# Kernel tuning notes

Measured on AMD Instinct MI355X. Metric: run time of the kernel, lower is better.

## Reference

```python
import jax, jax.numpy as jnp
import numpy as np

B, T, I, O = 64, 1024, 512, 512
EPS = 1e-5


def setup_inputs() -> dict:
    key = jax.random.key(0)
    k1, k2 = jax.random.split(key)
    x = jax.random.normal(k1, (B, T, I), dtype=jnp.float32)
    W = jax.random.normal(k2, (4 * O, I + O), dtype=jnp.float32) * 0.02
    gamma = jnp.ones((4, O), dtype=jnp.float32)
    beta = jnp.zeros((4, O), dtype=jnp.float32)
    init_hx = jnp.zeros((1, O), dtype=jnp.float32)
    init_cx = jnp.zeros((1, O), dtype=jnp.float32)
    return {"x": x, "W": W, "gamma": gamma, "beta": beta,
            "init_hx": init_hx, "init_cx": init_cx}


def reference(x, W, gamma, beta, init_hx, init_cx):
    b = x.shape[0]
    o = init_hx.shape[-1]

    def step(carry, xt):
        h, c = carry
        # fused gate projection: [B, I+O] @ [I+O, 4O] -> [B, 4, O]
        z = jnp.concatenate([xt, h], axis=-1) @ W.T
        z = z.reshape(b, 4, o)
        # LayerNorm over the last TWO dims (gate axis + feature axis), per torch nn.LayerNorm([4, O])
        mu = jnp.mean(z, axis=(-2, -1), keepdims=True)
        var = jnp.var(z, axis=(-2, -1), keepdims=True)
        zn = (z - mu) * jax.lax.rsqrt(var + EPS) * gamma + beta
        gates = jax.nn.sigmoid(zn[:, :3])  # f, i, o gates
        f_g, i_g, o_g = gates[:, 0], gates[:, 1], gates[:, 2]
        h_state = jax.nn.gelu(zn[:, 3], approximate=False)  # dropout = identity (eval)
        c_new = f_g * c + i_g * h_state
        h_new = o_g * c_new
        return (h_new, c_new), h_new

    h0 = jnp.broadcast_to(init_hx, (b, o))
    c0 = jnp.broadcast_to(init_cx, (b, o))
    x_t = jnp.swapaxes(x, 0, 1)  # [T, B, I]
    _, hs = jax.lax.scan(step, (h0, c0), x_t)
    return jnp.swapaxes(hs, 0, 1)  # [B, T, O]
```

## Files before the change

### kernel.cpp

```cpp
#include <hip/hip_runtime.h>
#include <math.h>

#define B_  64
#define T_  1024
#define I_  512
#define O_  512
#define NZ  2048
#define KW  1024
#define EPS 1e-5f

#define SREC 32
#define OSL  16

typedef short bf8_t  __attribute__((ext_vector_type(8)));
typedef float f32x4  __attribute__((ext_vector_type(4)));

__device__ __forceinline__ unsigned short f2bf(float f) {
  union { float f; unsigned u; } v; v.f = f;
  unsigned r = v.u + 0x7FFFu + ((v.u >> 16) & 1u);
  return (unsigned short)(r >> 16);
}
__device__ __forceinline__ float bf2f(unsigned short b) {
  union { unsigned u; float f; } v; v.u = ((unsigned)b) << 16;
  return v.f;
}

__global__ __launch_bounds__(256) void init_all(
    const float* __restrict__ init_hx,
    unsigned short* __restrict__ h, unsigned* __restrict__ sync) {
  int idx = blockIdx.x * 256 + threadIdx.x;
  if (idx < 2048) sync[idx] = 0u;
  if (idx < B_ * O_) h[idx] = f2bf(init_hx[idx & (O_ - 1)]);
}

__global__ __launch_bounds__(256) void wx_bf16(
    const float* __restrict__ W, unsigned short* __restrict__ Wbf) {
  int idx = blockIdx.x * 256 + threadIdx.x;
  int n  = idx >> 7;
  int k4 = (idx & 127) * 4;
  float4 v = *(const float4*)(W + (size_t)n * KW + k4);
  unsigned short* d = Wbf + (size_t)n * 512 + k4;
  d[0] = f2bf(v.x); d[1] = f2bf(v.y); d[2] = f2bf(v.z); d[3] = f2bf(v.w);
}

__global__ __launch_bounds__(256) void zx_gemm(
    const float* __restrict__ x, const unsigned short* __restrict__ Wbf,
    unsigned short* __restrict__ zx) {
  __shared__ unsigned short xl[64 * 520];

  const int tid  = threadIdx.x;
  const int w    = tid >> 6;
  const int lane = tid & 63;
  const int q    = lane >> 4;
  const int col  = lane & 15;
  const int m0   = blockIdx.x * 64;

  for (int e4 = tid; e4 < 64 * 128; e4 += 256) {
    int r  = e4 >> 7;
    int k4 = (e4 & 127) * 4;
    float4 v = *(const float4*)(x + (size_t)(m0 + r) * I_ + k4);
    unsigned short* d = &xl[r * 520 + k4];
    d[0] = f2bf(v.x); d[1] = f2bf(v.y); d[2] = f2bf(v.z); d[3] = f2bf(v.w);
  }
  __syncthreads();

  const unsigned short* __restrict__ arow = &xl[(16 * w + col) * 520];

  for (int nblk = 0; nblk < 32; ++nblk) {
    const int n0 = nblk * 64;
    f32x4 acc[4];
    #pragma unroll
    for (int i = 0; i < 4; ++i) acc[i] = (f32x4){0.f, 0.f, 0.f, 0.f};

    #pragma unroll
    for (int ks = 0; ks < 16; ++ks) {
      const int k0 = ks * 32 + q * 8;
      bf8_t af = *(const bf8_t*)(arow + k0);
      #pragma unroll
      for (int nt = 0; nt < 4; ++nt) {
        bf8_t bfr = *(const bf8_t*)(Wbf + (size_t)(n0 + nt * 16 + col) * 512 + k0);
        acc[nt] = __builtin_amdgcn_mfma_f32_16x16x32_bf16(af, bfr, acc[nt], 0, 0, 0);
      }
    }
    #pragma unroll
    for (int nt = 0; nt < 4; ++nt)
      #pragma unroll
      for (int r = 0; r < 4; ++r) {
        int m = m0 + 16 * w + 4 * q + r;
        zx[(size_t)m * NZ + n0 + nt * 16 + col] = f2bf(acc[nt][r]);
      }
  }
}

__global__ __launch_bounds__(256) void lstm_rec(
    const float* __restrict__ W, const float* __restrict__ gamma,
    const float* __restrict__ beta, const float* __restrict__ init_cx,
    const unsigned short* __restrict__ zx, unsigned short* __restrict__ h,
    unsigned long long* __restrict__ part8, float* __restrict__ out,
    unsigned* __restrict__ flags) {

  __shared__ unsigned short whlds[64 * 520];

  const int tid  = threadIdx.x;
  const int w    = tid >> 6;
  const int lane = tid & 63;
  const int q    = lane >> 4;
  const int col  = lane & 15;
  const int s    = blockIdx.x;
  const int o    = s * OSL + col;

  for (int e4 = tid; e4 < 64 * 128; e4 += 256) {
    int r  = e4 >> 7;
    int k4 = (e4 & 127) * 4;
    int g  = r >> 4, np = r & 15;
    const float4 v =
        *(const float4*)(W + (size_t)(512 * g + OSL * s + np) * KW + I_ + k4);
    unsigned short* d = &whlds[r * 520 + k4];
    d[0] = f2bf(v.x); d[1] = f2bf(v.y); d[2] = f2bf(v.z); d[3] = f2bf(v.w);
  }

  float gma[4], bta[4], c_reg[4];
  #pragma unroll
  for (int g = 0; g < 4; ++g) { gma[g] = gamma[g * O_ + o]; bta[g] = beta[g * O_ + o]; }
  { float c0 = init_cx[o];
    #pragma unroll
    for (int r = 0; r < 4; ++r) c_reg[r] = c0; }

  unsigned short zxl[16];
  #pragma unroll
  for (int g = 0; g < 4; ++g)
    #pragma unroll
    for (int r = 0; r < 4; ++r) {
      int b = 16 * w + 4 * q + r;
      zxl[g * 4 + r] = zx[((size_t)b * T_ + 0) * NZ + g * O_ + OSL * s + col];
    }

  __syncthreads();

  for (int t = 0; t < T_; ++t) {
    unsigned long long araw[32];
    const unsigned short* hrow = h + (16 * w + col) * O_;
    #pragma unroll
    for (int ks = 0; ks < 16; ++ks) {
      const unsigned long long* p =
          (const unsigned long long*)(hrow + ks * 32 + q * 8);
      araw[2 * ks]     = __hip_atomic_load(p,     __ATOMIC_RELAXED, __HIP_MEMORY_SCOPE_AGENT);
      araw[2 * ks + 1] = __hip_atomic_load(p + 1, __ATOMIC_RELAXED, __HIP_MEMORY_SCOPE_AGENT);
    }

    f32x4 acc[4];
    #pragma unroll
    for (int g = 0; g < 4; ++g) acc[g] = (f32x4){0.f, 0.f, 0.f, 0.f};

    #pragma unroll
    for (int ks = 0; ks < 16; ++ks) {
      union { unsigned long long u[2]; bf8_t v; } au;
      au.u[0] = araw[2 * ks]; au.u[1] = araw[2 * ks + 1];
      #pragma unroll
      for (int g = 0; g < 4; ++g) {
        bf8_t bfr = *(const bf8_t*)(&whlds[(g * 16 + col) * 520 + ks * 32 + q * 8]);
        acc[g] = __builtin_amdgcn_mfma_f32_16x16x32_bf16(au.v, bfr, acc[g], 0, 0, 0);
      }
    }

    float z[16];
    float s1[4], s2[4];
    #pragma unroll
    for (int r = 0; r < 4; ++r) { s1[r] = 0.f; s2[r] = 0.f; }
    #pragma unroll
    for (int g = 0; g < 4; ++g)
      #pragma unroll
      for (int r = 0; r < 4; ++r) {
        float zv = acc[g][r] + bf2f(zxl[g * 4 + r]);
        z[g * 4 + r] = zv;
        s1[r] += zv;
        s2[r] += zv * zv;
      }
    #pragma unroll
    for (int m = 1; m < 16; m <<= 1) {
      #pragma unroll
      for (int r = 0; r < 4; ++r) {
        s1[r] += __shfl_xor(s1[r], m, 64);
        s2[r] += __shfl_xor(s2[r], m, 64);
      }
    }
    if (col == 0) {
      #pragma unroll
      for (int r = 0; r < 4; ++r) {
        int b = 16 * w + 4 * q + r;
        union { float f[2]; unsigned long long u; } pv;
        pv.f[0] = s1[r]; pv.f[1] = s2[r];
        __hip_atomic_store(&part8[(size_t)s * 64 + b], pv.u,
                           __ATOMIC_RELAXED, __HIP_MEMORY_SCOPE_AGENT);
      }
    }

    __syncthreads();
    {
      const unsigned tgt = 2u * (unsigned)t + 1u;
      if (tid == 0)
        __hip_atomic_store(&flags[s * 16], tgt,
                           __ATOMIC_RELAXED, __HIP_MEMORY_SCOPE_AGENT);
      const unsigned* fp = &flags[(tid & 31) * 16];
      while (__hip_atomic_load(fp, __ATOMIC_RELAXED, __HIP_MEMORY_SCOPE_AGENT) < tgt) {}
    }

    float S1 = 0.f, S2 = 0.f;
    {
      const int brow = 16 * w + (lane & 15);
      const int sbase = (lane >> 4) * 8;
      #pragma unroll
      for (int i = 0; i < 8; ++i) {
        union { float f[2]; unsigned long long u; } pv;
        pv.u = __hip_atomic_load(&part8[(size_t)(sbase + i) * 64 + brow],
                                 __ATOMIC_RELAXED, __HIP_MEMORY_SCOPE_AGENT);
        S1 += pv.f[0]; S2 += pv.f[1];
      }
    }
    S1 += __shfl_xor(S1, 16, 64); S2 += __shfl_xor(S2, 16, 64);
    S1 += __shfl_xor(S1, 32, 64); S2 += __shfl_xor(S2, 32, 64);
    float mean_l = S1 * (1.f / NZ);
    float rstd_l = rsqrtf(S2 * (1.f / NZ) - mean_l * mean_l + EPS);

    float hnl[4];
    #pragma unroll
    for (int r = 0; r < 4; ++r) {
      int b = 16 * w + 4 * q + r;
      float mean = __shfl(mean_l, 4 * q + r, 64);
      float rstd = __shfl(rstd_l, 4 * q + r, 64);
      float zn0 = (z[0 * 4 + r] - mean) * rstd * gma[0] + bta[0];
      float zn1 = (z[1 * 4 + r] - mean) * rstd * gma[1] + bta[1];
      float zn2 = (z[2 * 4 + r] - mean) * rstd * gma[2] + bta[2];
      float zn3 = (z[3 * 4 + r] - mean) * rstd * gma[3] + bta[3];
      float fg = 1.f / (1.f + expf(-zn0));
      float ig = 1.f / (1.f + expf(-zn1));
      float og = 1.f / (1.f + expf(-zn2));
      float gg = 0.5f * zn3 * (1.f + erff(zn3 * 0.70710678118654752f));
      float cn = fg * c_reg[r] + ig * gg;
      float hn = og * cn;
      c_reg[r] = cn;
      hnl[r] = hn;
      __hip_atomic_store(&h[b * O_ + o], f2bf(hn),
                         __ATOMIC_RELAXED, __HIP_MEMORY_SCOPE_AGENT);
    }

    if (t + 1 < T_) {
      __syncthreads();
      const unsigned tgt = 2u * (unsigned)t + 2u;
      if (tid == 0)
        __hip_atomic_store(&flags[s * 16], tgt,
                           __ATOMIC_RELAXED, __HIP_MEMORY_SCOPE_AGENT);
      #pragma unroll
      for (int r = 0; r < 4; ++r) {
        int b = 16 * w + 4 * q + r;
        out[((size_t)b * T_ + t) * O_ + o] = hnl[r];
      }
      #pragma unroll
      for (int g = 0; g < 4; ++g)
        #pragma unroll
        for (int r = 0; r < 4; ++r) {
          int b = 16 * w + 4 * q + r;
          zxl[g * 4 + r] =
              zx[((size_t)b * T_ + (t + 1)) * NZ + g * O_ + OSL * s + col];
        }
      const unsigned* fp = &flags[(tid & 31) * 16];
      while (__hip_atomic_load(fp, __ATOMIC_RELAXED, __HIP_MEMORY_SCOPE_AGENT) < tgt) {}
    } else {
      #pragma unroll
      for (int r = 0; r < 4; ++r) {
        int b = 16 * w + 4 * q + r;
        out[((size_t)b * T_ + t) * O_ + o] = hnl[r];
      }
    }
  }
}

extern "C" void kernel_launch(void* const* d_in, const int* in_sizes, int n_in,
                              void* d_out, int out_size, void* d_ws, size_t ws_size,
                              hipStream_t stream) {
  const float* x       = (const float*)d_in[0];
  const float* W       = (const float*)d_in[1];
  const float* gamma   = (const float*)d_in[2];
  const float* beta    = (const float*)d_in[3];
  const float* init_hx = (const float*)d_in[4];
  const float* init_cx = (const float*)d_in[5];
  float* out = (float*)d_out;
  (void)in_sizes; (void)n_in; (void)out_size; (void)ws_size;

  char* ws = (char*)d_ws;
  unsigned*           flags = (unsigned*)(ws);
  unsigned long long* part8 = (unsigned long long*)(ws + 8192);
  unsigned short*     h     = (unsigned short*)(ws + 32768);
  unsigned short*     Wbf   = (unsigned short*)(ws + (1 << 20));
  unsigned short*     zx    = (unsigned short*)(ws + (4 << 20));

  init_all<<<128, 256, 0, stream>>>(init_hx, h, flags);
  wx_bf16<<<1024, 256, 0, stream>>>(W, Wbf);
  zx_gemm<<<1024, 256, 0, stream>>>(x, Wbf, zx);
  lstm_rec<<<SREC, 256, 0, stream>>>(W, gamma, beta, init_cx, zx, h, part8, out, flags);
}
```

Measured before the change: 9.486 ms.

## Fuse input projection into recurrent kernel, drop precomputed zx GEMM

Removes the separate zx_gemm pass and its bf16 zx buffer of B*T*2048 elements. Each recurrent block now keeps its slice of W_x in shared memory and computes the x-projection per timestep with extra MFMAs, after converting x to bf16 in a small preprocessing kernel. This cuts a large GEMM and its global-memory writes and reads, but puts twice the MFMA work on the serial critical path of the 32-block recurrence. Shared memory per block doubles to about 133 KB.

Result: slower. 10.60 ms (+11.8%).

```diff
diff --git a/kernel.cpp b/kernel.cpp
--- a/kernel.cpp
+++ b/kernel.cpp
@@ -20,10 +20,6 @@
   unsigned r = v.u + 0x7FFFu + ((v.u >> 16) & 1u);
   return (unsigned short)(r >> 16);
 }
-__device__ __forceinline__ float bf2f(unsigned short b) {
-  union { unsigned u; float f; } v; v.u = ((unsigned)b) << 16;
-  return v.f;
-}
 
 __global__ __launch_bounds__(256) void init_all(
     const float* __restrict__ init_hx,
@@ -33,73 +29,24 @@
   if (idx < B_ * O_) h[idx] = f2bf(init_hx[idx & (O_ - 1)]);
 }
 
-__global__ __launch_bounds__(256) void wx_bf16(
-    const float* __restrict__ W, unsigned short* __restrict__ Wbf) {
+__global__ __launch_bounds__(256) void x_bf16(
+    const float* __restrict__ x, unsigned short* __restrict__ xb) {
   int idx = blockIdx.x * 256 + threadIdx.x;
-  int n  = idx >> 7;
-  int k4 = (idx & 127) * 4;
-  float4 v = *(const float4*)(W + (size_t)n * KW + k4);
-  unsigned short* d = Wbf + (size_t)n * 512 + k4;
+  size_t base = (size_t)idx * 4;
+  float4 v = *(const float4*)(x + base);
+  unsigned short* d = xb + base;
   d[0] = f2bf(v.x); d[1] = f2bf(v.y); d[2] = f2bf(v.z); d[3] = f2bf(v.w);
 }
 
-__global__ __launch_bounds__(256) void zx_gemm(
-    const float* __restrict__ x, const unsigned short* __restrict__ Wbf,
-    unsigned short* __restrict__ zx) {
-  __shared__ unsigned short xl[64 * 520];
-
-  const int tid  = threadIdx.x;
-  const int w    = tid >> 6;
-  const int lane = tid & 63;
-  const int q    = lane >> 4;
-  const int col  = lane & 15;
-  const int m0   = blockIdx.x * 64;
-
-  for (int e4 = tid; e4 < 64 * 128; e4 += 256) {
-    int r  = e4 >> 7;
-    int k4 = (e4 & 127) * 4;
-    float4 v = *(const float4*)(x + (size_t)(m0 + r) * I_ + k4);
-    unsigned short* d = &xl[r * 520 + k4];
-    d[0] = f2bf(v.x); d[1] = f2bf(v.y); d[2] = f2bf(v.z); d[3] = f2bf(v.w);
-  }
-  __syncthreads();
-
-  const unsigned short* __restrict__ arow = &xl[(16 * w + col) * 520];
-
-  for (int nblk = 0; nblk < 32; ++nblk) {
-    const int n0 = nblk * 64;
-    f32x4 acc[4];
-    #pragma unroll
-    for (int i = 0; i < 4; ++i) acc[i] = (f32x4){0.f, 0.f, 0.f, 0.f};
-
-    #pragma unroll
-    for (int ks = 0; ks < 16; ++ks) {
-      const int k0 = ks * 32 + q * 8;
-      bf8_t af = *(const bf8_t*)(arow + k0);
-      #pragma unroll
-      for (int nt = 0; nt < 4; ++nt) {
-        bf8_t bfr = *(const bf8_t*)(Wbf + (size_t)(n0 + nt * 16 + col) * 512 + k0);
-        acc[nt] = __builtin_amdgcn_mfma_f32_16x16x32_bf16(af, bfr, acc[nt], 0, 0, 0);
-      }
-    }
-    #pragma unroll
-    for (int nt = 0; nt < 4; ++nt)
-      #pragma unroll
-      for (int r = 0; r < 4; ++r) {
-        int m = m0 + 16 * w + 4 * q + r;
-        zx[(size_t)m * NZ + n0 + nt * 16 + col] = f2bf(acc[nt][r]);
-      }
-  }
-}
-
-__global__ __launch_bounds__(256) void lstm_rec(
+__global__ __launch_bounds__(256, 1) void lstm_rec(
     const float* __restrict__ W, const float* __restrict__ gamma,
     const float* __restrict__ beta, const float* __restrict__ init_cx,
-    const unsigned short* __restrict__ zx, unsigned short* __restrict__ h,
+    const unsigned short* __restrict__ xb, unsigned short* __restrict__ h,
     unsigned long long* __restrict__ part8, float* __restrict__ out,
     unsigned* __restrict__ flags) {
 
   __shared__ unsigned short whlds[64 * 520];
+  __shared__ unsigned short wxlds[64 * 520];
 
   const int tid  = threadIdx.x;
   const int w    = tid >> 6;
@@ -113,10 +60,13 @@
     int r  = e4 >> 7;
     int k4 = (e4 & 127) * 4;
     int g  = r >> 4, np = r & 15;
-    const float4 v =
-        *(const float4*)(W + (size_t)(512 * g + OSL * s + np) * KW + I_ + k4);
-    unsigned short* d = &whlds[r * 520 + k4];
-    d[0] = f2bf(v.x); d[1] = f2bf(v.y); d[2] = f2bf(v.z); d[3] = f2bf(v.w);
+    const float* wrow = W + (size_t)(512 * g + OSL * s + np) * KW;
+    const float4 vh = *(const float4*)(wrow + I_ + k4);
+    unsigned short* dh = &whlds[r * 520 + k4];
+    dh[0] = f2bf(vh.x); dh[1] = f2bf(vh.y); dh[2] = f2bf(vh.z); dh[3] = f2bf(vh.w);
+    const float4 vx = *(const float4*)(wrow + k4);
+    unsigned short* dx = &wxlds[r * 520 + k4];
+    dx[0] = f2bf(vx.x); dx[1] = f2bf(vx.y); dx[2] = f2bf(vx.z); dx[3] = f2bf(vx.w);
   }
 
   float gma[4], bta[4], c_reg[4];
@@ -126,14 +76,16 @@
     #pragma unroll
     for (int r = 0; r < 4; ++r) c_reg[r] = c0; }
 
-  unsigned short zxl[16];
-  #pragma unroll
-  for (int g = 0; g < 4; ++g)
-    #pragma unroll
-    for (int r = 0; r < 4; ++r) {
-      int b = 16 * w + 4 * q + r;
-      zxl[g * 4 + r] = zx[((size_t)b * T_ + 0) * NZ + g * O_ + OSL * s + col];
-    }
+  unsigned long long xraw[32];
+  {
+    const unsigned short* xrow = xb + ((size_t)(16 * w + col) * T_ + 0) * I_ + q * 8;
+    #pragma unroll
+    for (int ks = 0; ks < 16; ++ks) {
+      const unsigned long long* p = (const unsigned long long*)(xrow + ks * 32);
+      xraw[2 * ks]     = p[0];
+      xraw[2 * ks + 1] = p[1];
+    }
+  }
 
   __syncthreads();
 
@@ -154,6 +106,17 @@
 
     #pragma unroll
     for (int ks = 0; ks < 16; ++ks) {
+      union { unsigned long long u[2]; bf8_t v; } xu;
+      xu.u[0] = xraw[2 * ks]; xu.u[1] = xraw[2 * ks + 1];
+      #pragma unroll
+      for (int g = 0; g < 4; ++g) {
+        bf8_t bfr = *(const bf8_t*)(&wxlds[(g * 16 + col) * 520 + ks * 32 + q * 8]);
+        acc[g] = __builtin_amdgcn_mfma_f32_16x16x32_bf16(xu.v, bfr, acc[g], 0, 0, 0);
+      }
+    }
+
+    #pragma unroll
+    for (int ks = 0; ks < 16; ++ks) {
       union { unsigned long long u[2]; bf8_t v; } au;
       au.u[0] = araw[2 * ks]; au.u[1] = araw[2 * ks + 1];
       #pragma unroll
@@ -171,7 +134,7 @@
     for (int g = 0; g < 4; ++g)
       #pragma unroll
       for (int r = 0; r < 4; ++r) {
-        float zv = acc[g][r] + bf2f(zxl[g * 4 + r]);
+        float zv = acc[g][r];
         z[g * 4 + r] = zv;
         s1[r] += zv;
         s2[r] += zv * zv;
@@ -255,14 +218,16 @@
         int b = 16 * w + 4 * q + r;
         out[((size_t)b * T_ + t) * O_ + o] = hnl[r];
       }
-      #pragma unroll
-      for (int g = 0; g < 4; ++g)
+      {
+        const unsigned short* xrow =
+            xb + ((size_t)(16 * w + col) * T_ + (t + 1)) * I_ + q * 8;
         #pragma unroll
-        for (int r = 0; r < 4; ++r) {
-          int b = 16 * w + 4 * q + r;
-          zxl[g * 4 + r] =
-              zx[((size_t)b * T_ + (t + 1)) * NZ + g * O_ + OSL * s + col];
+        for (int ks = 0; ks < 16; ++ks) {
+          const unsigned long long* p = (const unsigned long long*)(xrow + ks * 32);
+          xraw[2 * ks]     = p[0];
+          xraw[2 * ks + 1] = p[1];
         }
+      }
       const unsigned* fp = &flags[(tid & 31) * 16];
       while (__hip_atomic_load(fp, __ATOMIC_RELAXED, __HIP_MEMORY_SCOPE_AGENT) < tgt) {}
     } else {
@@ -291,11 +256,9 @@
   unsigned*           flags = (unsigned*)(ws);
   unsigned long long* part8 = (unsigned long long*)(ws + 8192);
   unsigned short*     h     = (unsigned short*)(ws + 32768);
-  unsigned short*     Wbf   = (unsigned short*)(ws + (1 << 20));
-  unsigned short*     zx    = (unsigned short*)(ws + (4 << 20));
+  unsigned short*     xbf   = (unsigned short*)(ws + (1 << 20));
 
   init_all<<<128, 256, 0, stream>>>(init_hx, h, flags);
-  wx_bf16<<<1024, 256, 0, stream>>>(W, Wbf);
-  zx_gemm<<<1024, 256, 0, stream>>>(x, Wbf, zx);
-  lstm_rec<<<SREC, 256, 0, stream>>>(W, gamma, beta, init_cx, zx, h, part8, out, flags);
-}
+  x_bf16<<<32768, 256, 0, stream>>>(x, xbf);
+  lstm_rec<<<SREC, 256, 0, stream>>>(W, gamma, beta, init_cx, xbf, h, part8, out, flags);
+}
```
